# Optimization experiments

Measured on AMD Instinct MI355X. Metric: run time of the kernel, lower is better.

The kernel has to match this reference:

```python
import jax, jax.numpy as jnp
import numpy as np

T, B, D_POSE, H, K_CODES = 30, 1024, 135, 512, 512
EPS = 1e-5


def _bn_relu(x, g, b):
    # BatchNorm1d (training-mode batch stats, biased var) + ReLU; x: (B, C, L)
    m = x.mean(axis=(0, 2), keepdims=True)
    v = x.var(axis=(0, 2), keepdims=True)
    y = g[None, :, None] * (x - m) * jax.lax.rsqrt(v + EPS) + b[None, :, None]
    return jax.nn.relu(y)


def _conv_sk(x, w):
    # Conv1d with stride == kernel_size (non-overlapping): pure reshaped GEMM.
    # x: (B, I, L), w: (O, I, K) torch layout -> (B, O, L//K)
    Bn, I, L = x.shape
    O, _, K = w.shape
    xr = x.reshape(Bn, I, L // K, K)
    return jnp.einsum('bitk,oik->bot', xr, w)


def _convT_sk(x, w):
    # ConvTranspose1d with stride == kernel_size: x (B, I, L), w (I, O, K) torch layout
    Bn, I, L = x.shape
    _, O, K = w.shape
    return jnp.einsum('bil,iok->bolk', x, w).reshape(Bn, O, L * K)


def setup_inputs() -> dict:
    key = jax.random.key(0)
    ks = jax.random.split(key, 12)
    sc = 0.05
    inp = {
        'input_seqs': jax.random.normal(ks[0], (T, B, D_POSE), jnp.float32),
        'W_in': jax.random.normal(ks[1], (D_POSE, H), jnp.float32) * sc,
        'b_in': jnp.zeros((H,), jnp.float32),
        'w_e1': jax.random.normal(ks[2], (H, H, 5), jnp.float32) * sc,
        'g_e1': jnp.ones((H,), jnp.float32), 'b_e1': jnp.zeros((H,), jnp.float32),
        'w_e2': jax.random.normal(ks[3], (H, H, 3), jnp.float32) * sc,
        'g_e2': jnp.ones((H,), jnp.float32), 'b_e2': jnp.zeros((H,), jnp.float32),
        'w_e3': jax.random.normal(ks[4], (H, H, 2), jnp.float32) * sc,
        'g_e3': jnp.ones((H,), jnp.float32), 'b_e3': jnp.zeros((H,), jnp.float32),
        'codebook': jax.random.normal(ks[5], (K_CODES, H), jnp.float32) * sc,
        'W_q': jax.random.normal(ks[6], (H, H), jnp.float32) * sc,
        'b_q': jnp.zeros((H,), jnp.float32),
        'w_d1': jax.random.normal(ks[7], (H, H, 2), jnp.float32) * sc,
        'g_d1': jnp.ones((H,), jnp.float32), 'b_d1': jnp.zeros((H,), jnp.float32),
        'w_d2': jax.random.normal(ks[8], (H, H, 3), jnp.float32) * sc,
        'g_d2': jnp.ones((H,), jnp.float32), 'b_d2': jnp.zeros((H,), jnp.float32),
        'w_d3': jax.random.normal(ks[9], (H, H, 5), jnp.float32) * sc,
        'g_d3': jnp.ones((H,), jnp.float32), 'b_d3': jnp.zeros((H,), jnp.float32),
        'W_out': jax.random.normal(ks[10], (H, D_POSE), jnp.float32) * sc,
        'b_out': jnp.zeros((D_POSE,), jnp.float32),
    }
    return inp


def reference(input_seqs, W_in, b_in, w_e1, g_e1, b_e1, w_e2, g_e2, b_e2,
              w_e3, g_e3, b_e3, codebook, W_q, b_q,
              w_d1, g_d1, b_d1, w_d2, g_d2, b_d2, w_d3, g_d3, b_d3,
              W_out, b_out):
    commitment_cost = 0.25
    # ---- EncoderCNN ----
    h = input_seqs @ W_in + b_in              # (T, B, H)
    h = jnp.transpose(h, (1, 2, 0))           # (B, H, T)
    h = _bn_relu(_conv_sk(h, w_e1), g_e1, b_e1)   # (B, H, 6)
    h = _bn_relu(_conv_sk(h, w_e2), g_e2, b_e2)   # (B, H, 2)
    z = _bn_relu(_conv_sk(h, w_e3), g_e3, b_e3)   # (B, H, 1)

    # ---- VQ (VQ_Payam, straight-through) ----
    Bn, D, L = z.shape
    flat = jnp.transpose(z, (0, 2, 1)).reshape(-1, D)            # (B*L, D)
    dist = (jnp.sum(flat ** 2, axis=1, keepdims=True)
            + jnp.sum(codebook ** 2, axis=1)
            - 2.0 * flat @ codebook.T)                           # (B*L, K)
    idx = jnp.argmin(dist, axis=1)                               # (B*L,)
    quantized = codebook[idx]                                    # (B*L, D)
    e_latent_loss = jnp.mean((jax.lax.stop_gradient(quantized) - flat) ** 2)
    q_latent_loss = jnp.mean((quantized - jax.lax.stop_gradient(flat)) ** 2)
    vq_loss = q_latent_loss + commitment_cost * e_latent_loss
    q_st = flat + jax.lax.stop_gradient(quantized - flat)        # straight-through
    avg_probs = jnp.mean(jax.nn.one_hot(idx, K_CODES, dtype=flat.dtype), axis=0)
    perplexity = jnp.exp(-jnp.sum(avg_probs * jnp.log(avg_probs + 1e-10)))

    # ---- DecoderCNN ----
    d = q_st @ W_q + b_q                      # (B, H)
    d = d[:, :, None]                         # (B, H, 1)
    d = _bn_relu(_convT_sk(d, w_d1), g_d1, b_d1)  # (B, H, 2)
    d = _bn_relu(_convT_sk(d, w_d2), g_d2, b_d2)  # (B, H, 6)
    d = _bn_relu(_convT_sk(d, w_d3), g_d3, b_d3)  # (B, H, 30)
    recon = jnp.transpose(d, (0, 2, 1)) @ W_out + b_out           # (B, T, D_POSE)
    return recon, vq_loss, perplexity
```

## Files before the change

### kernel.cpp

```cpp
#include <hip/hip_runtime.h>
#include <math.h>


typedef __attribute__((ext_vector_type(8))) short bf16x8;
typedef __attribute__((ext_vector_type(4))) float f32x4;

__device__ __forceinline__ unsigned pk_bf16(float a, float b) {
    unsigned ua = __float_as_uint(a), ub = __float_as_uint(b);
    ua += 0x7fffu + ((ua >> 16) & 1u);
    ub += 0x7fffu + ((ub >> 16) & 1u);
    return (ua >> 16) | (ub & 0xffff0000u);
}
__device__ __forceinline__ unsigned short bfh(float x) {
    unsigned u = __float_as_uint(x);
    u += 0x7fffu + ((u >> 16) & 1u);
    return (unsigned short)(u >> 16);
}
__device__ __forceinline__ float bf2f(unsigned short h) {
    return __uint_as_float(((unsigned)h) << 16);
}

__device__ __forceinline__ void gload16(const unsigned short* g, unsigned short* l) {
    __builtin_amdgcn_global_load_lds(
        (const __attribute__((address_space(1))) unsigned int*)g,
        (__attribute__((address_space(3))) unsigned int*)l, 16, 0, 0);
}

__device__ __forceinline__ void bn4(float4& a, const float* __restrict__ s,
                                    const float* __restrict__ c) {
    float4 sv = *(const float4*)s;
    float4 cv = *(const float4*)c;
    a.x = fmaxf(fmaf(a.x, sv.x, cv.x), 0.f);
    a.y = fmaxf(fmaf(a.y, sv.y, cv.y), 0.f);
    a.z = fmaxf(fmaf(a.z, sv.z, cv.z), 0.f);
    a.w = fmaxf(fmaf(a.w, sv.w, cv.w), 0.f);
}

#define FBK  32
#define FSTR 36

__global__ __launch_bounds__(256)
void k_gemm(const float* __restrict__ Abase,
            const float* __restrict__ Wt,
            float* __restrict__ Cout,
            const float* __restrict__ bnS, const float* __restrict__ bnB,
            unsigned long long* __restrict__ amin,
            const float* __restrict__ codesq,
            int Mslice, int K, int N, int decK)
{
    __shared__ __align__(16) float As[FBK][FSTR];
    __shared__ __align__(16) float Bs[FBK][FSTR];

    const int tid = threadIdx.x;
    const int z  = blockIdx.z;
    const int n0 = blockIdx.x << 5;
    const int m0 = blockIdx.y << 5;
    const int ty = tid >> 4;
    const int tx = tid & 15;

    const int a_slice = z / decK, wk = z - a_slice * decK;
    const float* Ap = Abase + (size_t)a_slice * (size_t)Mslice * (size_t)K;
    const float* Wp = Wt    + (size_t)wk * (size_t)K * (size_t)N;

    const int sr  = tid >> 3;
    const int sc4 = (tid & 7) << 2;

    int mrow = m0 + sr;
    if (mrow > Mslice - 1) mrow = Mslice - 1;
    const float* Arow_p = Ap + (size_t)mrow * K;

    float acc[2][2];
    acc[0][0] = 0.f; acc[0][1] = 0.f; acc[1][0] = 0.f; acc[1][1] = 0.f;

    float4 pa = *(const float4*)(Arow_p + sc4);
    if (bnS != nullptr) bn4(pa, bnS + sc4, bnB + sc4);
    float4 pb = *(const float4*)(Wp + (size_t)sr * N + n0 + sc4);

    for (int k0 = 0; k0 < K; k0 += FBK) {
        __syncthreads();
        As[sc4 + 0][sr] = pa.x;
        As[sc4 + 1][sr] = pa.y;
        As[sc4 + 2][sr] = pa.z;
        As[sc4 + 3][sr] = pa.w;
        *(float4*)&Bs[sr][sc4] = pb;
        const int k0n = k0 + FBK;
        if (k0n < K) {
            pa = *(const float4*)(Arow_p + k0n + sc4);
            if (bnS != nullptr) bn4(pa, bnS + k0n + sc4, bnB + k0n + sc4);
            pb = *(const float4*)(Wp + (size_t)(k0n + sr) * N + n0 + sc4);
        }
        __syncthreads();
#pragma unroll
        for (int kk = 0; kk < FBK; ++kk) {
            float2 av = *(const float2*)&As[kk][ty << 1];
            float2 bv = *(const float2*)&Bs[kk][tx << 1];
            acc[0][0] = fmaf(av.x, bv.x, acc[0][0]);
            acc[0][1] = fmaf(av.x, bv.y, acc[0][1]);
            acc[1][0] = fmaf(av.y, bv.x, acc[1][0]);
            acc[1][1] = fmaf(av.y, bv.y, acc[1][1]);
        }
    }

    if (amin != nullptr) {
        float2 cq = *(const float2*)(codesq + n0 + (tx << 1));
#pragma unroll
        for (int i = 0; i < 2; ++i) {
            const int m = m0 + (ty << 1) + i;
            float d0 = cq.x - 2.f * acc[i][0];
            float d1 = cq.y - 2.f * acc[i][1];
            int bj = (d1 < d0) ? 1 : 0;
            float best = (d1 < d0) ? d1 : d0;
            unsigned u = __float_as_uint(best);
            u = (u & 0x80000000u) ? ~u : (u | 0x80000000u);
            unsigned long long key =
                ((unsigned long long)u << 32) | (unsigned)(n0 + (tx << 1) + bj);
#pragma unroll
            for (int off = 1; off < 16; off <<= 1) {
                unsigned long long o = __shfl_xor(key, off, 64);
                if (o < key) key = o;
            }
            if (tx == 0 && m < Mslice) atomicMin(&amin[m], key);
        }
        return;
    }

#pragma unroll
    for (int i = 0; i < 2; ++i) {
        const int m = m0 + (ty << 1) + i;
        if (m < Mslice) {
            float2 v = make_float2(acc[i][0], acc[i][1]);
            *(float2*)&Cout[((size_t)z * Mslice + m) * N + n0 + (tx << 1)] = v;
        }
    }
}

__global__ __launch_bounds__(256)
void k_mfma_g(const unsigned short* __restrict__ Abase,
              const unsigned short* __restrict__ Bt,
              unsigned short* __restrict__ Cb,
              float* __restrict__ operm,
              const float* __restrict__ bias,
              float* __restrict__ stats,
              int Mslice, int K, int N, int decK)
{
    __shared__ __align__(16) unsigned short As[128 * 64];
    __shared__ __align__(16) unsigned short Bs[128 * 64];
    __shared__ float colsum[128], colsq[128];

    const int tid  = threadIdx.x;
    const int lane = tid & 63;
    const int wave = tid >> 6;
    const int wm = (wave >> 1) << 6;
    const int wn = (wave & 1) << 6;
    const int z  = blockIdx.z;
    const int n0 = blockIdx.x << 7;
    const int m0 = blockIdx.y << 7;

    if (stats != nullptr && tid < 128) { colsum[tid] = 0.f; colsq[tid] = 0.f; }

    const int a_slice = z / decK, wk = z - a_slice * decK;
    const unsigned short* Ap = Abase + (size_t)a_slice * (size_t)Mslice * (size_t)K;
    const unsigned short* Bp = Bt + (size_t)wk * (size_t)N * (size_t)K;

    const int srow  = tid >> 3;
    const int selem = ((tid & 7) ^ (srow & 7)) << 3;
    const unsigned short* Asrc = Ap + (size_t)(m0 + srow) * K + selem;
    unsigned short* Adst = As + tid * 8;
    unsigned short* Bdst = Bs + tid * 8;

    size_t boff[4];
#pragma unroll
    for (int c = 0; c < 4; ++c) {
        int brow = n0 + srow + (c << 5);
        if (brow > N - 1) brow = N - 1;
        boff[c] = (size_t)brow * K + selem;
    }

    f32x4 acc[4][4];
#pragma unroll
    for (int i = 0; i < 4; ++i)
#pragma unroll
        for (int j = 0; j < 4; ++j) acc[i][j] = (f32x4){0.f, 0.f, 0.f, 0.f};

    const int lidx = lane & 15;
    const int lq   = lane >> 4;

    for (int k0 = 0; k0 < K; k0 += 64) {
        __syncthreads();
#pragma unroll
        for (int c = 0; c < 4; ++c) {
            gload16(Asrc + (size_t)(c << 5) * K + k0, Adst + (c << 11));
            gload16(Bp + boff[c] + k0, Bdst + (c << 11));
        }
        __syncthreads();
#pragma unroll
        for (int ks = 0; ks < 2; ++ks) {
            const int ub = (ks << 2) + lq;
            const int uo = (ub ^ (lidx & 7)) << 3;
            bf16x8 af[4], bfv[4];
#pragma unroll
            for (int t = 0; t < 4; ++t)
                af[t] = *(const bf16x8*)&As[((wm + (t << 4) + lidx) << 6) + uo];
#pragma unroll
            for (int t = 0; t < 4; ++t)
                bfv[t] = *(const bf16x8*)&Bs[((wn + (t << 4) + lidx) << 6) + uo];
#pragma unroll
            for (int mt = 0; mt < 4; ++mt)
#pragma unroll
                for (int nt = 0; nt < 4; ++nt)
                    acc[mt][nt] = __builtin_amdgcn_mfma_f32_16x16x32_bf16(
                        af[mt], bfv[nt], acc[mt][nt], 0, 0, 0);
        }
    }

    const int rbase = lq << 2;
#pragma unroll
    for (int nt = 0; nt < 4; ++nt) {
        const int col = n0 + wn + (nt << 4) + lidx;
        const float badd = (bias != nullptr && col < N) ? bias[col] : 0.f;
        float s = 0.f, q = 0.f;
#pragma unroll
        for (int mt = 0; mt < 4; ++mt) {
#pragma unroll
            for (int r = 0; r < 4; ++r) {
                float x = acc[mt][nt][r];
                s += x; q += x * x;
                const int row = m0 + wm + (mt << 4) + rbase + r;
                if (operm != nullptr) {
                    if (col < N) {
                        const int t = row >> 10, b = row & 1023;
                        operm[(size_t)b * 4050 + t * 135 + col] = x + badd;
                    }
                } else {
                    Cb[((size_t)z * Mslice + row) * (size_t)N + col] = bfh(x + badd);
                }
            }
        }
        if (stats != nullptr) {
            s += __shfl_xor(s, 16, 64); s += __shfl_xor(s, 32, 64);
            q += __shfl_xor(q, 16, 64); q += __shfl_xor(q, 32, 64);
            if (lq == 0) {
                atomicAdd(&colsum[wn + (nt << 4) + lidx], s);
                atomicAdd(&colsq [wn + (nt << 4) + lidx], q);
            }
        }
    }
    if (stats != nullptr) {
        __syncthreads();
        if (tid < 128) {
            atomicAdd(&stats[n0 + tid],       colsum[tid]);
            atomicAdd(&stats[512 + n0 + tid], colsq[tid]);
        }
    }
}

__global__ __launch_bounds__(256)
void k_b64g(const unsigned short* __restrict__ Abase,
            const unsigned short* __restrict__ Bt,
            unsigned short* __restrict__ Cb,
            const float* __restrict__ bias,
            float* __restrict__ stats,
            int Mslice, int K, int N, int decK)
{
    __shared__ __align__(16) unsigned short As[64 * 64];
    __shared__ __align__(16) unsigned short Bs[64 * 64];
    __shared__ float colsum[64], colsq[64];

    const int tid  = threadIdx.x;
    const int lane = tid & 63;
    const int wave = tid >> 6;
    const int wm = (wave >> 1) << 5;
    const int wn = (wave & 1) << 5;
    const int z  = blockIdx.z;
    const int n0 = blockIdx.x << 6;
    const int m0 = blockIdx.y << 6;

    if (stats != nullptr && tid < 64) { colsum[tid] = 0.f; colsq[tid] = 0.f; }

    const int a_slice = z / decK, wk = z - a_slice * decK;
    const unsigned short* Ap = Abase + (size_t)a_slice * (size_t)Mslice * (size_t)K;
    const unsigned short* Bp = Bt + (size_t)wk * (size_t)N * (size_t)K;

    const int srow  = tid >> 3;
    const int selem = ((tid & 7) ^ (srow & 7)) << 3;
    const unsigned short* Asrc = Ap + (size_t)(m0 + srow) * K + selem;
    const unsigned short* Bsrc = Bp + (size_t)(n0 + srow) * K + selem;
    unsigned short* Adst = As + tid * 8;
    unsigned short* Bdst = Bs + tid * 8;

    f32x4 acc[2][2];
#pragma unroll
    for (int i = 0; i < 2; ++i)
#pragma unroll
        for (int j = 0; j < 2; ++j) acc[i][j] = (f32x4){0.f, 0.f, 0.f, 0.f};

    const int lidx = lane & 15;
    const int lq   = lane >> 4;

    for (int k0 = 0; k0 < K; k0 += 64) {
        __syncthreads();
#pragma unroll
        for (int c = 0; c < 2; ++c) {
            gload16(Asrc + (size_t)(c << 5) * K + k0, Adst + (c << 11));
            gload16(Bsrc + (size_t)(c << 5) * K + k0, Bdst + (c << 11));
        }
        __syncthreads();
#pragma unroll
        for (int ks = 0; ks < 2; ++ks) {
            const int ub = (ks << 2) + lq;
            const int uo = (ub ^ (lidx & 7)) << 3;
            bf16x8 af[2], bfv[2];
#pragma unroll
            for (int t = 0; t < 2; ++t)
                af[t] = *(const bf16x8*)&As[((wm + (t << 4) + lidx) << 6) + uo];
#pragma unroll
            for (int t = 0; t < 2; ++t)
                bfv[t] = *(const bf16x8*)&Bs[((wn + (t << 4) + lidx) << 6) + uo];
#pragma unroll
            for (int mt = 0; mt < 2; ++mt)
#pragma unroll
                for (int nt = 0; nt < 2; ++nt)
                    acc[mt][nt] = __builtin_amdgcn_mfma_f32_16x16x32_bf16(
                        af[mt], bfv[nt], acc[mt][nt], 0, 0, 0);
        }
    }

    const int rbase = lq << 2;
#pragma unroll
    for (int nt = 0; nt < 2; ++nt) {
        const int col = n0 + wn + (nt << 4) + lidx;
        const float badd = (bias != nullptr) ? bias[col] : 0.f;
        float s = 0.f, q = 0.f;
#pragma unroll
        for (int mt = 0; mt < 2; ++mt) {
#pragma unroll
            for (int r = 0; r < 4; ++r) {
                float x = acc[mt][nt][r];
                s += x; q += x * x;
                const int row = m0 + wm + (mt << 4) + rbase + r;
                Cb[((size_t)z * Mslice + row) * (size_t)N + col] = bfh(x + badd);
            }
        }
        if (stats != nullptr) {
            s += __shfl_xor(s, 16, 64); s += __shfl_xor(s, 32, 64);
            q += __shfl_xor(q, 16, 64); q += __shfl_xor(q, 32, 64);
            if (lq == 0) {
                atomicAdd(&colsum[wn + (nt << 4) + lidx], s);
                atomicAdd(&colsq [wn + (nt << 4) + lidx], q);
            }
        }
    }
    if (stats != nullptr) {
        __syncthreads();
        if (tid < 64) {
            atomicAdd(&stats[n0 + tid],       colsum[tid]);
            atomicAdd(&stats[512 + n0 + tid], colsq[tid]);
        }
    }
}

__global__ __launch_bounds__(256)
void k_sp64g(const unsigned short* __restrict__ Ahg,
             const unsigned short* __restrict__ Alg,
             const unsigned short* __restrict__ Whi,
             const unsigned short* __restrict__ Wlo,
             float* __restrict__ Cout, float* __restrict__ stats,
             int Mslice, int Kp, int N, int n_terms)
{
    __shared__ __align__(16) unsigned short Ah[64 * 32];
    __shared__ __align__(16) unsigned short Al[64 * 32];
    __shared__ __align__(16) unsigned short Bh[64 * 32];
    __shared__ __align__(16) unsigned short Bl[64 * 32];
    __shared__ float colsum[64], colsq[64];

    const int tid  = threadIdx.x;
    const int lane = tid & 63;
    const int wave = tid >> 6;
    const int wm = (wave >> 1) << 5;
    const int wn = (wave & 1) << 5;
    const int z  = blockIdx.z;
    const int n0 = blockIdx.x << 6;
    const int m0 = blockIdx.y << 6;

    if (stats != nullptr && tid < 64) { colsum[tid] = 0.f; colsq[tid] = 0.f; }

    const int srow  = tid >> 2;
    const int selem = ((tid & 3) ^ (srow & 3)) << 3;
    unsigned short* Ahd = Ah + tid * 8;
    unsigned short* Ald = Al + tid * 8;
    unsigned short* Bhd = Bh + tid * 8;
    unsigned short* Bld = Bl + tid * 8;

    f32x4 acc[2][2];
#pragma unroll
    for (int i = 0; i < 2; ++i)
#pragma unroll
        for (int j = 0; j < 2; ++j) acc[i][j] = (f32x4){0.f, 0.f, 0.f, 0.f};

    const int lidx = lane & 15;
    const int lq   = lane >> 4;
    const int uo   = (lq ^ (lidx & 3)) << 3;

    const int cpk = Kp >> 5;
    const int tot = n_terms * cpk;

    int lt = 0, lk = 0;
    for (int c = 0; c < tot; ++c) {
        __syncthreads();
        {
            const size_t ab = ((size_t)(z * n_terms + lt) * Mslice + m0 + srow)
                              * (size_t)Kp + lk + selem;
            const size_t bb = ((size_t)lt * N + n0 + srow) * (size_t)Kp + lk + selem;
            gload16(Ahg + ab, Ahd);
            gload16(Alg + ab, Ald);
            gload16(Whi + bb, Bhd);
            gload16(Wlo + bb, Bld);
        }
        lk += 32; if (lk >= Kp) { lk = 0; ++lt; }
        __syncthreads();
        bf16x8 ah[2], al[2], bh[2], bl[2];
#pragma unroll
        for (int t = 0; t < 2; ++t) {
            const int ra = ((wm + (t << 4) + lidx) << 5) + uo;
            ah[t] = *(const bf16x8*)&Ah[ra];
            al[t] = *(const bf16x8*)&Al[ra];
        }
#pragma unroll
        for (int t = 0; t < 2; ++t) {
            const int rb = ((wn + (t << 4) + lidx) << 5) + uo;
            bh[t] = *(const bf16x8*)&Bh[rb];
            bl[t] = *(const bf16x8*)&Bl[rb];
        }
#pragma unroll
        for (int mt = 0; mt < 2; ++mt)
#pragma unroll
            for (int nt = 0; nt < 2; ++nt) {
                acc[mt][nt] = __builtin_amdgcn_mfma_f32_16x16x32_bf16(
                    ah[mt], bh[nt], acc[mt][nt], 0, 0, 0);
                acc[mt][nt] = __builtin_amdgcn_mfma_f32_16x16x32_bf16(
                    al[mt], bh[nt], acc[mt][nt], 0, 0, 0);
                acc[mt][nt] = __builtin_amdgcn_mfma_f32_16x16x32_bf16(
                    ah[mt], bl[nt], acc[mt][nt], 0, 0, 0);
            }
    }

    const int rbase = lq << 2;
#pragma unroll
    for (int nt = 0; nt < 2; ++nt) {
        const int col = n0 + wn + (nt << 4) + lidx;
        float s = 0.f, q = 0.f;
#pragma unroll
        for (int mt = 0; mt < 2; ++mt) {
#pragma unroll
            for (int r = 0; r < 4; ++r) {
                float x = acc[mt][nt][r];
                s += x; q += x * x;
                const int row = m0 + wm + (mt << 4) + rbase + r;
                Cout[((size_t)z * Mslice + row) * (size_t)N + col] = x;
            }
        }
        if (stats != nullptr) {
            s += __shfl_xor(s, 16, 64); s += __shfl_xor(s, 32, 64);
            q += __shfl_xor(q, 16, 64); q += __shfl_xor(q, 32, 64);
            if (lq == 0) {
                atomicAdd(&colsum[wn + (nt << 4) + lidx], s);
                atomicAdd(&colsq [wn + (nt << 4) + lidx], q);
            }
        }
    }
    if (stats != nullptr) {
        __syncthreads();
        if (tid < 64) {
            atomicAdd(&stats[n0 + tid],       colsum[tid]);
            atomicAdd(&stats[512 + n0 + tid], colsq[tid]);
        }
    }
}

__global__ void k_prep(float* __restrict__ zbase, unsigned long long* __restrict__ amin,
                       const float* __restrict__ codebook, float* __restrict__ codeT,
                       float* __restrict__ codesq,
                       const float* __restrict__ w_e2, unsigned short* __restrict__ whi_e2,
                       unsigned short* __restrict__ wlo_e2,
                       const float* __restrict__ w_e3, unsigned short* __restrict__ whi_e3,
                       unsigned short* __restrict__ wlo_e3,
                       const float* __restrict__ W_q,  unsigned short* __restrict__ wqb,
                       const float* __restrict__ w_d1, unsigned short* __restrict__ wd1b,
                       const float* __restrict__ w_d2, unsigned short* __restrict__ wd2b,
                       const float* __restrict__ w_d3, unsigned short* __restrict__ wd3b,
                       const float* __restrict__ W_out, unsigned short* __restrict__ woutb,
                       const float* __restrict__ in_seqs,
                       unsigned short* __restrict__ in_h, unsigned short* __restrict__ in_l)
{
    __shared__ float red[4];
    const int bid = blockIdx.x;
    const int tid = threadIdx.x;

    if (bid < 32) {
        int t = bid * 256 + tid;
        if (t < 6720) zbase[t] = 0.f;
        if (t < 1024) amin[t] = ~0ULL;
        return;
    }
    if (bid < 1056) {
        int idx = (bid - 32) * 256 + tid;
        int i = (idx >> 9) & 511, o = idx & 511;
        codeT[idx] = codebook[(o << 9) + i];
        return;
    }
    if (bid < 1568) {
        int c = bid - 1056;
        float s = 0.f;
        for (int i = tid; i < 512; i += 256) { float v = codebook[c * 512 + i]; s += v * v; }
        for (int off = 32; off; off >>= 1) s += __shfl_down(s, off, 64);
        if ((tid & 63) == 0) red[tid >> 6] = s;
        __syncthreads();
        if (tid == 0) codesq[c] = red[0] + red[1] + red[2] + red[3];
        return;
    }
    if (bid < 4640) {
        int idx = (bid - 1568) * 256 + tid;
        int i = idx & 511, o = (idx >> 9) & 511, k = idx >> 18;
        float v = w_e2[(((o << 9) + i) * 3) + k];
        unsigned short h = bfh(v);
        whi_e2[idx] = h; wlo_e2[idx] = bfh(v - bf2f(h));
        return;
    }
    if (bid < 6688) {
        int idx = (bid - 4640) * 256 + tid;
        int i = idx & 511, o = (idx >> 9) & 511, k = idx >> 18;
        float v = w_e3[(((o << 9) + i) * 2) + k];
        unsigned short h = bfh(v);
        whi_e3[idx] = h; wlo_e3[idx] = bfh(v - bf2f(h));
        return;
    }
    if (bid < 7712) {
        int idx = (bid - 6688) * 256 + tid;
        int i = idx & 511, o = (idx >> 9) & 511;
        wqb[idx] = bfh(W_q[((size_t)i << 9) + o]);
        return;
    }
    if (bid < 9760) {
        int idx = (bid - 7712) * 256 + tid;
        int i = idx & 511, o = (idx >> 9) & 511, k = idx >> 18;
        wd1b[idx] = bfh(w_d1[(((size_t)i << 9) + o) * 2 + k]);
        return;
    }
    if (bid < 12832) {
        int idx = (bid - 9760) * 256 + tid;
        int i = idx & 511, o = (idx >> 9) & 511, k = idx >> 18;
        wd2b[idx] = bfh(w_d2[(((size_t)i << 9) + o) * 3 + k]);
        return;
    }
    if (bid < 17952) {
        int idx = (bid - 12832) * 256 + tid;
        int i = idx & 511, o = (idx >> 9) & 511, k = idx >> 18;
        wd3b[idx] = bfh(w_d3[(((size_t)i << 9) + o) * 5 + k]);
        return;
    }
    if (bid < 18222) {
        int idx = (bid - 17952) * 256 + tid;
        if (idx >= 69120) return;
        int i = idx % 512, o = idx / 512;
        woutb[idx] = bfh(W_out[((size_t)i * 135) + o]);
        return;
    }
    {
        int idx = (bid - 18222) * 256 + tid;
        if (idx >= 4915200) return;
        int i = idx % 160, r = idx / 160;
        float v = (i < 135) ? in_seqs[(size_t)r * 135 + i] : 0.f;
        unsigned short h = bfh(v);
        in_h[idx] = h; in_l[idx] = bfh(v - bf2f(h));
    }
}

__global__ void k_repack(const float* __restrict__ w, float* __restrict__ wt,
                         int Kc, int total)
{
    int idx = blockIdx.x * 256 + threadIdx.x;
    if (idx >= total) return;
    int k = idx >> 18;
    int rem = idx & 262143;
    int i = rem >> 9, o = rem & 511;
    wt[idx] = w[(((o << 9) + i) * Kc + k)];
}

__global__ void k_repack_sp_weff(const float* __restrict__ weff,
                                 unsigned short* __restrict__ whi,
                                 unsigned short* __restrict__ wlo,
                                 int total)
{
    int idx = blockIdx.x * 256 + threadIdx.x;
    if (idx >= total) return;
    int i = idx % 160;
    int o = (idx / 160) & 511;
    int t = idx / 81920;
    float v = (i < 135) ? weff[((size_t)t * 135 + i) * 512 + o] : 0.f;
    unsigned short h = bfh(v);
    whi[idx] = h;
    wlo[idx] = bfh(v - bf2f(h));
}

__global__ void k_bnsplit(const float* __restrict__ x,
                          const float* __restrict__ sc, const float* __restrict__ sh,
                          unsigned short* __restrict__ hq, unsigned short* __restrict__ lq_,
                          int total4)
{
    int idx = blockIdx.x * 256 + threadIdx.x;
    if (idx >= total4) return;
    const int base = idx << 2;
    float4 f = *(const float4*)(x + base);
    const int k = base & 511;
    float4 s = *(const float4*)(sc + k);
    float4 c = *(const float4*)(sh + k);
    float y0 = fmaxf(fmaf(f.x, s.x, c.x), 0.f);
    float y1 = fmaxf(fmaf(f.y, s.y, c.y), 0.f);
    float y2 = fmaxf(fmaf(f.z, s.z, c.z), 0.f);
    float y3 = fmaxf(fmaf(f.w, s.w, c.w), 0.f);
    unsigned short h0 = bfh(y0), h1 = bfh(y1), h2 = bfh(y2), h3 = bfh(y3);
    unsigned short l0 = bfh(y0 - bf2f(h0)), l1 = bfh(y1 - bf2f(h1));
    unsigned short l2 = bfh(y2 - bf2f(h2)), l3 = bfh(y3 - bf2f(h3));
    *(uint2*)&hq[base]  = make_uint2((unsigned)h0 | ((unsigned)h1 << 16),
                                     (unsigned)h2 | ((unsigned)h3 << 16));
    *(uint2*)&lq_[base] = make_uint2((unsigned)l0 | ((unsigned)l1 << 16),
                                     (unsigned)l2 | ((unsigned)l3 << 16));
}

__global__ void k_bnapply(const unsigned short* __restrict__ x,
                          const float* __restrict__ sc, const float* __restrict__ sh,
                          unsigned short* __restrict__ y, int total8)
{
    int idx = blockIdx.x * 256 + threadIdx.x;
    if (idx >= total8) return;
    const int base = idx << 3;
    uint4 raw = *(const uint4*)(x + base);
    const int k = base & 511;
    float4 s0 = *(const float4*)(sc + k);
    float4 c0 = *(const float4*)(sh + k);
    float4 s1 = *(const float4*)(sc + k + 4);
    float4 c1 = *(const float4*)(sh + k + 4);
    unsigned* u = (unsigned*)&raw;
    float x0 = __uint_as_float(u[0] << 16),        x1 = __uint_as_float(u[0] & 0xffff0000u);
    float x2 = __uint_as_float(u[1] << 16),        x3 = __uint_as_float(u[1] & 0xffff0000u);
    float x4 = __uint_as_float(u[2] << 16),        x5 = __uint_as_float(u[2] & 0xffff0000u);
    float x6 = __uint_as_float(u[3] << 16),        x7 = __uint_as_float(u[3] & 0xffff0000u);
    x0 = fmaxf(fmaf(x0, s0.x, c0.x), 0.f); x1 = fmaxf(fmaf(x1, s0.y, c0.y), 0.f);
    x2 = fmaxf(fmaf(x2, s0.z, c0.z), 0.f); x3 = fmaxf(fmaf(x3, s0.w, c0.w), 0.f);
    x4 = fmaxf(fmaf(x4, s1.x, c1.x), 0.f); x5 = fmaxf(fmaf(x5, s1.y, c1.y), 0.f);
    x6 = fmaxf(fmaf(x6, s1.z, c1.z), 0.f); x7 = fmaxf(fmaf(x7, s1.w, c1.w), 0.f);
    *(uint4*)&y[base] = make_uint4(pk_bf16(x0, x1), pk_bf16(x2, x3),
                                   pk_bf16(x4, x5), pk_bf16(x6, x7));
}

__global__ void k_bn_fin(const float* __restrict__ stats,
                         const float* __restrict__ g, const float* __restrict__ b,
                         float* __restrict__ sc, float* __restrict__ sh, float inv_n)
{
    int c = blockIdx.x * blockDim.x + threadIdx.x;
    if (c >= 512) return;
    float m = stats[c] * inv_n;
    float v = stats[512 + c] * inv_n - m * m;
    float a = (float)((double)g[c] / sqrt((double)v + 1e-5));
    sc[c] = a;
    sh[c] = b[c] - m * a;
}

__global__ void k_vq_gather(const unsigned long long* __restrict__ amin,
                            const float* __restrict__ codebook,
                            const float* __restrict__ e3pre,
                            const float* __restrict__ sc, const float* __restrict__ sh,
                            unsigned short* __restrict__ quant_bf,
                            float* __restrict__ loss,
                            unsigned int* __restrict__ hist)
{
    int b = blockIdx.x; int t = threadIdx.x;
    unsigned int idx = (unsigned int)(amin[b] & 0xFFFFFFFFull) & 511u;
    float part = 0.f;
    for (int i = t; i < 512; i += 256) {
        float q = codebook[(size_t)idx * 512 + i];
        quant_bf[(size_t)b * 512 + i] = bfh(q);
        float x = e3pre[(size_t)b * 512 + i];
        float f = fmaxf(fmaf(x, sc[i], sh[i]), 0.f);
        float d = q - f;
        part += d * d;
    }
    for (int off = 32; off; off >>= 1) part += __shfl_down(part, off, 64);
    __shared__ float red[4];
    if ((t & 63) == 0) red[t >> 6] = part;
    __syncthreads();
    if (t == 0) {
        atomicAdd(loss, red[0] + red[1] + red[2] + red[3]);
        atomicAdd(&hist[idx], 1u);
    }
}

__global__ void k_scalars(const unsigned int* __restrict__ hist,
                          const float* __restrict__ loss, float* __restrict__ out)
{
    int t = threadIdx.x;
    float p = (float)hist[t] * (1.0f / 1024.0f);
    float e = p * logf(p + 1e-10f);
    for (int off = 32; off; off >>= 1) e += __shfl_down(e, off, 64);
    __shared__ float red[8];
    if ((t & 63) == 0) red[t >> 6] = e;
    __syncthreads();
    if (t == 0) {
        float s = 0.f;
        for (int i = 0; i < 8; ++i) s += red[i];
        out[4147200] = 1.25f * loss[0] * (1.0f / 524288.0f);
        out[4147201] = expf(-s);
    }
}

extern "C" void kernel_launch(void* const* d_in, const int* in_sizes, int n_in,
                              void* d_out, int out_size, void* d_ws, size_t ws_size,
                              hipStream_t stream)
{
    const float* in_seqs = (const float*)d_in[0];
    const float* W_in  = (const float*)d_in[1];
    const float* w_e1  = (const float*)d_in[3];
    const float* g_e1  = (const float*)d_in[4];
    const float* be1   = (const float*)d_in[5];
    const float* w_e2  = (const float*)d_in[6];
    const float* g_e2  = (const float*)d_in[7];
    const float* be2   = (const float*)d_in[8];
    const float* w_e3  = (const float*)d_in[9];
    const float* g_e3  = (const float*)d_in[10];
    const float* be3   = (const float*)d_in[11];
    const float* codebook = (const float*)d_in[12];
    const float* W_q   = (const float*)d_in[13];
    const float* b_q   = (const float*)d_in[14];
    const float* w_d1  = (const float*)d_in[15];
    const float* g_d1  = (const float*)d_in[16];
    const float* bd1   = (const float*)d_in[17];
    const float* w_d2  = (const float*)d_in[18];
    const float* g_d2  = (const float*)d_in[19];
    const float* bd2   = (const float*)d_in[20];
    const float* w_d3  = (const float*)d_in[21];
    const float* g_d3  = (const float*)d_in[22];
    const float* bd3   = (const float*)d_in[23];
    const float* W_out = (const float*)d_in[24];
    const float* b_out = (const float*)d_in[25];
    float* out = (float*)d_out;

    float* W = (float*)d_ws;
    unsigned long long* amin = (unsigned long long*)W;
    float* stats  = W + 2048;
    float* lossp  = W + 8192;
    unsigned int* hist = (unsigned int*)(W + 8256);
    float* scsh   = W + 8768;
    float* codesq = W + 14912;
    float* wt_e1  = W + 15424;
    float* weff   = W + 1326144;
    float* codeT  = W + 1671744;
    unsigned short* esw = (unsigned short*)(W + 1933888);
    unsigned short* whi_e1 = esw;
    unsigned short* wlo_e1 = esw + 409600;
    unsigned short* whi_e2 = esw + 819200;
    unsigned short* wlo_e2 = esw + 1605632;
    unsigned short* whi_e3 = esw + 2392064;
    unsigned short* wlo_e3 = esw + 2916352;
    unsigned short* in_h  = (unsigned short*)(W + 3654208);
    unsigned short* in_l  = in_h + 4915200;
    unsigned short* d3pre = (unsigned short*)(W + 3654208);
    float* e1f = W + 11518528;
    unsigned short* e1h = (unsigned short*)(W + 14664256);
    unsigned short* e1l = e1h + 3145728;
    float* e2f = W + 17809984;
    unsigned short* e2h = (unsigned short*)(W + 18858560);
    unsigned short* e2l = e2h + 1048576;
    unsigned short* d2pre = (unsigned short*)(W + 17809984);
    unsigned short* d2bf  = d2pre + 3145728;
    float* e3f = W + 20955712;
    unsigned short* quant_bf = (unsigned short*)(W + 21480000);
    unsigned short* d0bf     = (unsigned short*)(W + 21742144);
    unsigned short* d1pre    = (unsigned short*)(W + 22004288);
    unsigned short* d1bf     = (unsigned short*)(W + 22528640);
    unsigned short* d3bf     = (unsigned short*)(W + 23052928);

    unsigned short* db    = (unsigned short*)wt_e1;
    unsigned short* wqb   = db;
    unsigned short* wd1b  = db + 262144;
    unsigned short* wd2b  = db + 786432;
    unsigned short* wd3b  = db + 1572864;
    unsigned short* woutb = db + 2883584;

    float* st_e1 = stats + 0 * 1024; float* sc_e1 = scsh + 0 * 1024; float* sh_e1 = sc_e1 + 512;
    float* st_e2 = stats + 1 * 1024; float* sc_e2 = scsh + 1 * 1024; float* sh_e2 = sc_e2 + 512;
    float* st_e3 = stats + 2 * 1024; float* sc_e3 = scsh + 2 * 1024; float* sh_e3 = sc_e3 + 512;
    float* st_d1 = stats + 3 * 1024; float* sc_d1 = scsh + 3 * 1024; float* sh_d1 = sc_d1 + 512;
    float* st_d2 = stats + 4 * 1024; float* sc_d2 = scsh + 4 * 1024; float* sh_d2 = sc_d2 + 512;
    float* st_d3 = stats + 5 * 1024; float* sc_d3 = scsh + 5 * 1024; float* sh_d3 = sc_d3 + 512;

    dim3 blk(256);

    k_repack<<<dim3(5 * 1024), blk, 0, stream>>>(w_e1, wt_e1, 5, 5 * 262144);
    k_gemm<<<dim3(16, 5, 5), blk, 0, stream>>>(W_in, wt_e1, weff,
        nullptr, nullptr, nullptr, nullptr, 135, 512, 512, 5);
    k_repack_sp_weff<<<dim3(1600), blk, 0, stream>>>(weff, whi_e1, wlo_e1, 409600);

    k_prep<<<dim3(37422), blk, 0, stream>>>(stats, amin,
        codebook, codeT, codesq,
        w_e2, whi_e2, wlo_e2, w_e3, whi_e3, wlo_e3,
        W_q, wqb, w_d1, wd1b, w_d2, wd2b, w_d3, wd3b, W_out, woutb,
        in_seqs, in_h, in_l);

    k_sp64g<<<dim3(8, 16, 6), blk, 0, stream>>>(in_h, in_l, whi_e1, wlo_e1,
        e1f, st_e1, 1024, 160, 512, 5);
    k_bn_fin<<<dim3(2), blk, 0, stream>>>(st_e1, g_e1, be1, sc_e1, sh_e1, 1.f / 6144.f);
    k_bnsplit<<<dim3(3072), blk, 0, stream>>>(e1f, sc_e1, sh_e1, e1h, e1l, 786432);

    k_sp64g<<<dim3(8, 16, 2), blk, 0, stream>>>(e1h, e1l, whi_e2, wlo_e2,
        e2f, st_e2, 1024, 512, 512, 3);
    k_bn_fin<<<dim3(2), blk, 0, stream>>>(st_e2, g_e2, be2, sc_e2, sh_e2, 1.f / 2048.f);
    k_bnsplit<<<dim3(1024), blk, 0, stream>>>(e2f, sc_e2, sh_e2, e2h, e2l, 262144);

    k_sp64g<<<dim3(8, 16, 1), blk, 0, stream>>>(e2h, e2l, whi_e3, wlo_e3,
        e3f, st_e3, 1024, 512, 512, 2);
    k_bn_fin<<<dim3(2), blk, 0, stream>>>(st_e3, g_e3, be3, sc_e3, sh_e3, 1.f / 1024.f);

    k_gemm<<<dim3(16, 32, 1), blk, 0, stream>>>(e3f, codeT, nullptr,
        sc_e3, sh_e3, amin, codesq, 1024, 512, 512, 1);
    k_vq_gather<<<dim3(1024), blk, 0, stream>>>(amin, codebook, e3f, sc_e3, sh_e3,
                                                quant_bf, lossp, hist);

    k_b64g<<<dim3(8, 16, 1), blk, 0, stream>>>(quant_bf, wqb, d0bf,
        b_q, nullptr, 1024, 512, 512, 1);

    k_b64g<<<dim3(8, 16, 2), blk, 0, stream>>>(d0bf, wd1b, d1pre,
        nullptr, st_d1, 1024, 512, 512, 2);
    k_bn_fin<<<dim3(2), blk, 0, stream>>>(st_d1, g_d1, bd1, sc_d1, sh_d1, 1.f / 2048.f);
    k_bnapply<<<dim3(512), blk, 0, stream>>>(d1pre, sc_d1, sh_d1, d1bf, 131072);

    k_b64g<<<dim3(8, 16, 6), blk, 0, stream>>>(d1bf, wd2b, d2pre,
        nullptr, st_d2, 1024, 512, 512, 3);
    k_bn_fin<<<dim3(2), blk, 0, stream>>>(st_d2, g_d2, bd2, sc_d2, sh_d2, 1.f / 6144.f);
    k_bnapply<<<dim3(1536), blk, 0, stream>>>(d2pre, sc_d2, sh_d2, d2bf, 393216);

    k_mfma_g<<<dim3(4, 8, 30), blk, 0, stream>>>(d2bf, wd3b, d3pre,
        nullptr, nullptr, st_d3, 1024, 512, 512, 5);
    k_bn_fin<<<dim3(2), blk, 0, stream>>>(st_d3, g_d3, bd3, sc_d3, sh_d3, 1.f / 30720.f);
    k_bnapply<<<dim3(7680), blk, 0, stream>>>(d3pre, sc_d3, sh_d3, d3bf, 1966080);

    k_mfma_g<<<dim3(2, 240, 1), blk, 0, stream>>>(d3bf, woutb, nullptr,
        out, b_out, nullptr, 30720, 512, 135, 1);

    k_scalars<<<dim3(1), dim3(512), 0, stream>>>(hist, lossp, out);
}
```

Measured before the change: 442.6 us.

## Double-buffer LDS tiles in GEMM kernels to overlap global loads with MFMA

Converts the three MFMA GEMM kernels (128x128, 64x64, and split-precision 64x64) from single-buffered LDS staging with two barriers per k-step to a double-buffered scheme. Each kernel prefetches the next k-tile into the alternate buffer via global_load_lds while computing on the current one, leaving one barrier per step. This aims to hide global-memory latency behind matrix math, at the cost of doubled LDS use. That may reduce occupancy, especially for the 128x128 kernel at 64KB.

```diff
diff --git a/kernel.cpp b/kernel.cpp
--- a/kernel.cpp
+++ b/kernel.cpp
@@ -143,8 +143,8 @@
               float* __restrict__ stats,
               int Mslice, int K, int N, int decK)
 {
-    __shared__ __align__(16) unsigned short As[128 * 64];
-    __shared__ __align__(16) unsigned short Bs[128 * 64];
+    __shared__ __align__(16) unsigned short As[2][128 * 64];
+    __shared__ __align__(16) unsigned short Bs[2][128 * 64];
     __shared__ float colsum[128], colsq[128];
 
     const int tid  = threadIdx.x;
@@ -165,8 +165,6 @@
     const int srow  = tid >> 3;
     const int selem = ((tid & 7) ^ (srow & 7)) << 3;
     const unsigned short* Asrc = Ap + (size_t)(m0 + srow) * K + selem;
-    unsigned short* Adst = As + tid * 8;
-    unsigned short* Bdst = Bs + tid * 8;
 
     size_t boff[4];
 #pragma unroll
@@ -185,25 +183,37 @@
     const int lidx = lane & 15;
     const int lq   = lane >> 4;
 
-    for (int k0 = 0; k0 < K; k0 += 64) {
-        __syncthreads();
-#pragma unroll
-        for (int c = 0; c < 4; ++c) {
-            gload16(Asrc + (size_t)(c << 5) * K + k0, Adst + (c << 11));
-            gload16(Bp + boff[c] + k0, Bdst + (c << 11));
-        }
-        __syncthreads();
+#pragma unroll
+    for (int c = 0; c < 4; ++c) {
+        gload16(Asrc + (size_t)(c << 5) * K, &As[0][tid * 8 + (c << 11)]);
+        gload16(Bp + boff[c],                &Bs[0][tid * 8 + (c << 11)]);
+    }
+    __syncthreads();
+
+    const int nsteps = K >> 6;
+    int cur = 0;
+    for (int t = 0; t < nsteps; ++t) {
+        if (t + 1 < nsteps) {
+            const int k0n = (t + 1) << 6;
+#pragma unroll
+            for (int c = 0; c < 4; ++c) {
+                gload16(Asrc + (size_t)(c << 5) * K + k0n,
+                        &As[cur ^ 1][tid * 8 + (c << 11)]);
+                gload16(Bp + boff[c] + k0n,
+                        &Bs[cur ^ 1][tid * 8 + (c << 11)]);
+            }
+        }
 #pragma unroll
         for (int ks = 0; ks < 2; ++ks) {
             const int ub = (ks << 2) + lq;
             const int uo = (ub ^ (lidx & 7)) << 3;
             bf16x8 af[4], bfv[4];
 #pragma unroll
-            for (int t = 0; t < 4; ++t)
-                af[t] = *(const bf16x8*)&As[((wm + (t << 4) + lidx) << 6) + uo];
-#pragma unroll
-            for (int t = 0; t < 4; ++t)
-                bfv[t] = *(const bf16x8*)&Bs[((wn + (t << 4) + lidx) << 6) + uo];
+            for (int t4 = 0; t4 < 4; ++t4)
+                af[t4] = *(const bf16x8*)&As[cur][((wm + (t4 << 4) + lidx) << 6) + uo];
+#pragma unroll
+            for (int t4 = 0; t4 < 4; ++t4)
+                bfv[t4] = *(const bf16x8*)&Bs[cur][((wn + (t4 << 4) + lidx) << 6) + uo];
 #pragma unroll
             for (int mt = 0; mt < 4; ++mt)
 #pragma unroll
@@ -211,6 +221,8 @@
                     acc[mt][nt] = __builtin_amdgcn_mfma_f32_16x16x32_bf16(
                         af[mt], bfv[nt], acc[mt][nt], 0, 0, 0);
         }
+        __syncthreads();
+        cur ^= 1;
     }
 
     const int rbase = lq << 2;
@@ -262,8 +274,8 @@
             float* __restrict__ stats,
             int Mslice, int K, int N, int decK)
 {
-    __shared__ __align__(16) unsigned short As[64 * 64];
-    __shared__ __align__(16) unsigned short Bs[64 * 64];
+    __shared__ __align__(16) unsigned short As[2][64 * 64];
+    __shared__ __align__(16) unsigned short Bs[2][64 * 64];
     __shared__ float colsum[64], colsq[64];
 
     const int tid  = threadIdx.x;
@@ -285,8 +297,6 @@
     const int selem = ((tid & 7) ^ (srow & 7)) << 3;
     const unsigned short* Asrc = Ap + (size_t)(m0 + srow) * K + selem;
     const unsigned short* Bsrc = Bp + (size_t)(n0 + srow) * K + selem;
-    unsigned short* Adst = As + tid * 8;
-    unsigned short* Bdst = Bs + tid * 8;
 
     f32x4 acc[2][2];
 #pragma unroll
@@ -297,25 +307,37 @@
     const int lidx = lane & 15;
     const int lq   = lane >> 4;
 
-    for (int k0 = 0; k0 < K; k0 += 64) {
-        __syncthreads();
-#pragma unroll
-        for (int c = 0; c < 2; ++c) {
-            gload16(Asrc + (size_t)(c << 5) * K + k0, Adst + (c << 11));
-            gload16(Bsrc + (size_t)(c << 5) * K + k0, Bdst + (c << 11));
-        }
-        __syncthreads();
+#pragma unroll
+    for (int c = 0; c < 2; ++c) {
+        gload16(Asrc + (size_t)(c << 5) * K, &As[0][tid * 8 + (c << 11)]);
+        gload16(Bsrc + (size_t)(c << 5) * K, &Bs[0][tid * 8 + (c << 11)]);
+    }
+    __syncthreads();
+
+    const int nsteps = K >> 6;
+    int cur = 0;
+    for (int t = 0; t < nsteps; ++t) {
+        if (t + 1 < nsteps) {
+            const int k0n = (t + 1) << 6;
+#pragma unroll
+            for (int c = 0; c < 2; ++c) {
+                gload16(Asrc + (size_t)(c << 5) * K + k0n,
+                        &As[cur ^ 1][tid * 8 + (c << 11)]);
+                gload16(Bsrc + (size_t)(c << 5) * K + k0n,
+                        &Bs[cur ^ 1][tid * 8 + (c << 11)]);
+            }
+        }
 #pragma unroll
         for (int ks = 0; ks < 2; ++ks) {
             const int ub = (ks << 2) + lq;
             const int uo = (ub ^ (lidx & 7)) << 3;
             bf16x8 af[2], bfv[2];
 #pragma unroll
-            for (int t = 0; t < 2; ++t)
-                af[t] = *(const bf16x8*)&As[((wm + (t << 4) + lidx) << 6) + uo];
-#pragma unroll
-            for (int t = 0; t < 2; ++t)
-                bfv[t] = *(const bf16x8*)&Bs[((wn + (t << 4) + lidx) << 6) + uo];
+            for (int t2 = 0; t2 < 2; ++t2)
+                af[t2] = *(const bf16x8*)&As[cur][((wm + (t2 << 4) + lidx) << 6) + uo];
+#pragma unroll
+            for (int t2 = 0; t2 < 2; ++t2)
+                bfv[t2] = *(const bf16x8*)&Bs[cur][((wn + (t2 << 4) + lidx) << 6) + uo];
 #pragma unroll
             for (int mt = 0; mt < 2; ++mt)
 #pragma unroll
@@ -323,6 +345,8 @@
                     acc[mt][nt] = __builtin_amdgcn_mfma_f32_16x16x32_bf16(
                         af[mt], bfv[nt], acc[mt][nt], 0, 0, 0);
         }
+        __syncthreads();
+        cur ^= 1;
     }
 
     const int rbase = lq << 2;
@@ -367,10 +391,10 @@
              float* __restrict__ Cout, float* __restrict__ stats,
              int Mslice, int Kp, int N, int n_terms)
 {
-    __shared__ __align__(16) unsigned short Ah[64 * 32];
-    __shared__ __align__(16) unsigned short Al[64 * 32];
-    __shared__ __align__(16) unsigned short Bh[64 * 32];
-    __shared__ __align__(16) unsigned short Bl[64 * 32];
+    __shared__ __align__(16) unsigned short Ah[2][64 * 32];
+    __shared__ __align__(16) unsigned short Al[2][64 * 32];
+    __shared__ __align__(16) unsigned short Bh[2][64 * 32];
+    __shared__ __align__(16) unsigned short Bl[2][64 * 32];
     __shared__ float colsum[64], colsq[64];
 
     const int tid  = threadIdx.x;
@@ -386,10 +410,6 @@
 
     const int srow  = tid >> 2;
     const int selem = ((tid & 3) ^ (srow & 3)) << 3;
-    unsigned short* Ahd = Ah + tid * 8;
-    unsigned short* Ald = Al + tid * 8;
-    unsigned short* Bhd = Bh + tid * 8;
-    unsigned short* Bld = Bl + tid * 8;
 
     f32x4 acc[2][2];
 #pragma unroll
@@ -404,32 +424,43 @@
     const int cpk = Kp >> 5;
     const int tot = n_terms * cpk;
 
-    int lt = 0, lk = 0;
+    {
+        const size_t ab = ((size_t)(z * n_terms) * Mslice + m0 + srow)
+                          * (size_t)Kp + selem;
+        const size_t bb = ((size_t)(n0 + srow)) * (size_t)Kp + selem;
+        gload16(Ahg + ab, &Ah[0][tid * 8]);
+        gload16(Alg + ab, &Al[0][tid * 8]);
+        gload16(Whi + bb, &Bh[0][tid * 8]);
+        gload16(Wlo + bb, &Bl[0][tid * 8]);
+    }
+    __syncthreads();
+
+    int cur = 0;
+    int lt = 0, lk = 32;
+    if (lk >= Kp) { lk = 0; lt = 1; }
     for (int c = 0; c < tot; ++c) {
-        __syncthreads();
-        {
+        if (c + 1 < tot) {
             const size_t ab = ((size_t)(z * n_terms + lt) * Mslice + m0 + srow)
                               * (size_t)Kp + lk + selem;
             const size_t bb = ((size_t)lt * N + n0 + srow) * (size_t)Kp + lk + selem;
-            gload16(Ahg + ab, Ahd);
-            gload16(Alg + ab, Ald);
-            gload16(Whi + bb, Bhd);
-            gload16(Wlo + bb, Bld);
-        }
-        lk += 32; if (lk >= Kp) { lk = 0; ++lt; }
-        __syncthreads();
+            gload16(Ahg + ab, &Ah[cur ^ 1][tid * 8]);
+            gload16(Alg + ab, &Al[cur ^ 1][tid * 8]);
+            gload16(Whi + bb, &Bh[cur ^ 1][tid * 8]);
+            gload16(Wlo + bb, &Bl[cur ^ 1][tid * 8]);
+            lk += 32; if (lk >= Kp) { lk = 0; ++lt; }
+        }
         bf16x8 ah[2], al[2], bh[2], bl[2];
 #pragma unroll
         for (int t = 0; t < 2; ++t) {
             const int ra = ((wm + (t << 4) + lidx) << 5) + uo;
-            ah[t] = *(const bf16x8*)&Ah[ra];
-            al[t] = *(const bf16x8*)&Al[ra];
+            ah[t] = *(const bf16x8*)&Ah[cur][ra];
+            al[t] = *(const bf16x8*)&Al[cur][ra];
         }
 #pragma unroll
         for (int t = 0; t < 2; ++t) {
             const int rb = ((wn + (t << 4) + lidx) << 5) + uo;
-            bh[t] = *(const bf16x8*)&Bh[rb];
-            bl[t] = *(const bf16x8*)&Bl[rb];
+            bh[t] = *(const bf16x8*)&Bh[cur][rb];
+            bl[t] = *(const bf16x8*)&Bl[cur][rb];
         }
 #pragma unroll
         for (int mt = 0; mt < 2; ++mt)
@@ -442,6 +473,8 @@
                 acc[mt][nt] = __builtin_amdgcn_mfma_f32_16x16x32_bf16(
                     ah[mt], bl[nt], acc[mt][nt], 0, 0, 0);
             }
+        __syncthreads();
+        cur ^= 1;
     }
 
     const int rbase = lq << 2;
```

Result: faster. 425.0 us (-4.0%).
